# Kernel tuning notes

Hardware: AMD Instinct MI355X
Metric: run time of the kernel (lower is better)

## Reference

```python
import jax, jax.numpy as jnp
import numpy as np

TAU = 2.0   # membrane decay time constant
TH = 1.0    # firing threshold

N, T, D = 64, 64, 8192


def setup_inputs() -> dict:
    key = jax.random.key(0)
    k1, k2, k3 = jax.random.split(key, 3)
    x = jax.random.normal(k1, (N, T, D), dtype=jnp.float32)
    momentum = jax.random.uniform(k2, (1,), dtype=jnp.float32)
    lamb = jax.random.uniform(k3, (1,), dtype=jnp.float32)
    return {"x": x, "momentum": momentum, "lamb": lamb}


def reference(x, momentum, lamb):
    """Momentum LIF neuron scanned over the time axis.

    Assumed dynamics (CUDA kernel source unavailable; reduces to standard
    STBP hard-reset LIF when momentum == 0 and lamb == 0):
        v_t = momentum * v_{t-1} + x_t - lamb * u_{t-1}   # momentum on input current
        u_t = (1 - 1/tau) * u_{t-1} + v_t                 # leaky integrate
        s_t = H(u_t - th)                                 # spike
        u_t = u_t * (1 - s_t)                             # hard reset
    x: [N, T, D] -> spikes: [N, T, D]
    """
    decay = 1.0 - 1.0 / TAU
    mom = momentum[0]
    lb = lamb[0]

    def step(carry, xt):
        u, v = carry                      # each [N, D]
        v = mom * v + xt - lb * u
        u = decay * u + v
        s = (u >= TH).astype(xt.dtype)
        u = u * (1.0 - s)                 # hard reset
        return (u, v), s

    xs = jnp.swapaxes(x, 0, 1)            # [T, N, D] for time scan
    u0 = jnp.zeros_like(x[:, 0])
    v0 = jnp.zeros_like(x[:, 0])
    _, spikes = jax.lax.scan(step, (u0, v0), xs)
    return jnp.swapaxes(spikes, 0, 1)      # [N, T, D]
```

## Files before the change

kernel.cpp:

```cpp
#include <hip/hip_runtime.h>
#include <stdint.h>


#define N_ 64
#define T_ 64
#define D_ 8192
#define PF 8
#define CPT 4

typedef __attribute__((ext_vector_type(4))) float f32x4;

__global__ __launch_bounds__(256) void lif_fused(
    const float* __restrict__ x,
    const float* __restrict__ momp,
    const float* __restrict__ lambp,
    float* __restrict__ out)
{
#pragma clang fp contract(off)
    float mom  = momp[0];
    float lamb = lambp[0];
    const float decay = 0.5f;

    asm volatile("" : "+s"(mom), "+s"(lamb));

    const int g  = blockIdx.x * blockDim.x + threadIdx.x;
    const int n  = g >> 11;
    const int dq = g & 2047;
    const size_t base = (size_t)n * (size_t)(T_ * D_) + ((size_t)dq << 2);

    const f32x4* __restrict__ xv = reinterpret_cast<const f32x4*>(x + base);
    f32x4* __restrict__ ov       = reinterpret_cast<f32x4*>(out + base);
    const int RS = D_ / 4;

    asm volatile("s_waitcnt vmcnt(0)" ::: "memory");

    f32x4 xs[PF];
#pragma unroll
    for (int i = 0; i < PF; ++i) {
        const f32x4* a = xv + (size_t)i * RS;
        asm volatile("global_load_dwordx4 %0, %1, off" : "=v"(xs[i]) : "v"(a));
    }

    float u[CPT] = {0.f, 0.f, 0.f, 0.f};
    float v[CPT] = {0.f, 0.f, 0.f, 0.f};
    uint32_t blo[CPT] = {0u, 0u, 0u, 0u};
    uint32_t bhi[CPT] = {0u, 0u, 0u, 0u};

#pragma unroll
    for (int t = 0; t < T_ - PF; ++t) {
        const int slot = t & (PF - 1);
        asm volatile("s_waitcnt vmcnt(7)" : "+v"(xs[slot]));
        const f32x4 xt = xs[slot];
        const f32x4* a = xv + (size_t)(t + PF) * RS;
        asm volatile("global_load_dwordx4 %0, %1, off" : "=v"(xs[slot]) : "v"(a));

#pragma unroll
        for (int c = 0; c < CPT; ++c) {
            const float t1 = mom * v[c];
            const float t2 = lamb * u[c];
            v[c] = (t1 + xt[c]) - t2;
            u[c] = decay * u[c] + v[c];
            const bool sp = (u[c] >= 1.0f);
            if (t < 32) blo[c] |= ((uint32_t)sp) << t;
            else        bhi[c] |= ((uint32_t)sp) << (t - 32);
            u[c] = sp ? 0.0f : u[c];
        }
    }

    asm volatile("s_waitcnt vmcnt(0)"
                 : "+v"(xs[0]), "+v"(xs[1]), "+v"(xs[2]), "+v"(xs[3]),
                   "+v"(xs[4]), "+v"(xs[5]), "+v"(xs[6]), "+v"(xs[7]));

#pragma unroll
    for (int t = T_ - PF; t < T_; ++t) {
        const f32x4 xt = xs[t & (PF - 1)];
#pragma unroll
        for (int c = 0; c < CPT; ++c) {
            const float t1 = mom * v[c];
            const float t2 = lamb * u[c];
            v[c] = (t1 + xt[c]) - t2;
            u[c] = decay * u[c] + v[c];
            const bool sp = (u[c] >= 1.0f);
            if (t < 32) blo[c] |= ((uint32_t)sp) << t;
            else        bhi[c] |= ((uint32_t)sp) << (t - 32);
            u[c] = sp ? 0.0f : u[c];
        }
    }

#pragma unroll
    for (int t = 0; t < T_; ++t) {
        f32x4 o;
#pragma unroll
        for (int c = 0; c < CPT; ++c) {
            const uint32_t w = (t < 32) ? blo[c] : bhi[c];
            o[c] = ((w >> (t & 31)) & 1u) ? 1.0f : 0.0f;
        }
        __builtin_nontemporal_store(o, ov + (size_t)t * RS);
    }
}

extern "C" void kernel_launch(void* const* d_in, const int* in_sizes, int n_in,
                              void* d_out, int out_size, void* d_ws, size_t ws_size,
                              hipStream_t stream) {
    const float* x    = (const float*)d_in[0];
    const float* momp = (const float*)d_in[1];
    const float* lamb = (const float*)d_in[2];
    float* out = (float*)d_out;

    dim3 block(256);
    dim3 grid((N_ * D_ / CPT) / 256);
    hipLaunchKernelGGL(lif_fused, grid, block, 0, stream, x, momp, lamb, out);
}
```

Baseline: 248.9 us.

## Split LIF into bit-packed compute pass and separate contiguous expand kernel

The single fused kernel is split in two. The first computes the spike recurrence and writes one 64-bit spike mask per chain to workspace. The second kernel expands those masks into float outputs with fully contiguous stores. The first kernel also remaps block IDs to spread blocks across XCDs and adds a per-timestep workgroup barrier to keep waves in lockstep for load locality. The aim is to separate the strided output writes from the latency-bound scan, at the cost of an extra launch and a small workspace round trip.

```diff
diff --git a/kernel.cpp b/kernel.cpp
--- a/kernel.cpp
+++ b/kernel.cpp
@@ -10,11 +10,11 @@
 
 typedef __attribute__((ext_vector_type(4))) float f32x4;
 
-__global__ __launch_bounds__(256) void lif_fused(
+__global__ __launch_bounds__(256) void lif_compute_pack(
     const float* __restrict__ x,
     const float* __restrict__ momp,
     const float* __restrict__ lambp,
-    float* __restrict__ out)
+    uint2* __restrict__ ws)
 {
 #pragma clang fp contract(off)
     float mom  = momp[0];
@@ -23,13 +23,15 @@
 
     asm volatile("" : "+s"(mom), "+s"(lamb));
 
-    const int g  = blockIdx.x * blockDim.x + threadIdx.x;
+    const int bid  = (int)blockIdx.x;
+    const int lbid = (bid & 7) * 64 + (bid >> 3);
+
+    const int g  = lbid * 256 + (int)threadIdx.x;
     const int n  = g >> 11;
     const int dq = g & 2047;
     const size_t base = (size_t)n * (size_t)(T_ * D_) + ((size_t)dq << 2);
 
     const f32x4* __restrict__ xv = reinterpret_cast<const f32x4*>(x + base);
-    f32x4* __restrict__ ov       = reinterpret_cast<f32x4*>(out + base);
     const int RS = D_ / 4;
 
     asm volatile("s_waitcnt vmcnt(0)" ::: "memory");
@@ -65,6 +67,7 @@
             else        bhi[c] |= ((uint32_t)sp) << (t - 32);
             u[c] = sp ? 0.0f : u[c];
         }
+        __builtin_amdgcn_s_barrier();
     }
 
     asm volatile("s_waitcnt vmcnt(0)"
@@ -87,16 +90,39 @@
         }
     }
 
+    const int chain = (n << 13) + (dq << 2);
 #pragma unroll
-    for (int t = 0; t < T_; ++t) {
-        f32x4 o;
-#pragma unroll
-        for (int c = 0; c < CPT; ++c) {
-            const uint32_t w = (t < 32) ? blo[c] : bhi[c];
-            o[c] = ((w >> (t & 31)) & 1u) ? 1.0f : 0.0f;
-        }
-        __builtin_nontemporal_store(o, ov + (size_t)t * RS);
-    }
+    for (int c = 0; c < CPT; ++c)
+        ws[chain + c] = make_uint2(blo[c], bhi[c]);
+}
+
+__global__ __launch_bounds__(256) void lif_expand(
+    const uint2* __restrict__ ws,
+    float* __restrict__ out)
+{
+    const int g = blockIdx.x * blockDim.x + threadIdx.x;
+    const size_t e = (size_t)g << 2;
+    const int nt = (int)(e >> 13);
+    const int t  = nt & (T_ - 1);
+    const int n  = nt >> 6;
+    const int d  = (int)(e & (D_ - 1));
+    const int chain = (n << 13) + d;
+
+    const uint2 w0 = ws[chain + 0];
+    const uint2 w1 = ws[chain + 1];
+    const uint2 w2 = ws[chain + 2];
+    const uint2 w3 = ws[chain + 3];
+
+    const int  sh = t & 31;
+    const bool hi = (t >= 32);
+
+    f32x4 o;
+    o.x = (((hi ? w0.y : w0.x) >> sh) & 1u) ? 1.0f : 0.0f;
+    o.y = (((hi ? w1.y : w1.x) >> sh) & 1u) ? 1.0f : 0.0f;
+    o.z = (((hi ? w2.y : w2.x) >> sh) & 1u) ? 1.0f : 0.0f;
+    o.w = (((hi ? w3.y : w3.x) >> sh) & 1u) ? 1.0f : 0.0f;
+
+    __builtin_nontemporal_store(o, reinterpret_cast<f32x4*>(out) + g);
 }
 
 extern "C" void kernel_launch(void* const* d_in, const int* in_sizes, int n_in,
@@ -106,8 +132,17 @@
     const float* momp = (const float*)d_in[1];
     const float* lamb = (const float*)d_in[2];
     float* out = (float*)d_out;
+    uint2* ws  = (uint2*)d_ws;
 
-    dim3 block(256);
-    dim3 grid((N_ * D_ / CPT) / 256);
-    hipLaunchKernelGGL(lif_fused, grid, block, 0, stream, x, momp, lamb, out);
+    {
+        dim3 block(256);
+        dim3 grid((N_ * D_ / CPT) / 256);
+        hipLaunchKernelGGL(lif_compute_pack, grid, block, 0, stream,
+                           x, momp, lamb, ws);
+    }
+    {
+        dim3 block(256);
+        dim3 grid((N_ * T_ * D_ / 4) / 256);
+        hipLaunchKernelGGL(lif_expand, grid, block, 0, stream, ws, out);
+    }
 }
```

Result: faster. 236.5 us (-5.0%).
